# Kernel optimization log

Hardware: AMD Instinct MI355X
Metric: run time of the kernel (lower is better)

Reference implementation:

```python
import jax, jax.numpy as jnp
import numpy as np

B, D_IN, H, C = 8192, 3072, 2000, 10


def binarized(x):
    # deterministic Binarize: sign(x) scaled by mean |x| (matches quant_mode='det', allow_scale=True)
    return jnp.sign(x) * jnp.mean(jnp.abs(x))


def setup_inputs() -> dict:
    key = jax.random.key(0)
    ks = jax.random.split(key, 6)

    def lin(k, out_f, in_f):
        # torch nn.Linear default init: U(-1/sqrt(in_f), 1/sqrt(in_f))
        bound = 1.0 / np.sqrt(in_f)
        kw, kb = jax.random.split(k)
        W = jax.random.uniform(kw, (out_f, in_f), minval=-bound, maxval=bound, dtype=jnp.float32)
        b = jax.random.uniform(kb, (out_f,), minval=-bound, maxval=bound, dtype=jnp.float32)
        return W, b

    x = jax.random.normal(ks[0], (B, D_IN), dtype=jnp.float32)
    W1, b1 = lin(ks[1], H, D_IN)
    W2, b2 = lin(ks[2], H, H)
    W3, b3 = lin(ks[3], H, H)
    W4, b4 = lin(ks[4], H, H)
    W5, b5 = lin(ks[5], C, H)
    return {"x": x, "W1": W1, "b1": b1, "W2": W2, "b2": b2,
            "W3": W3, "b3": b3, "W4": W4, "b4": b4, "W5": W5, "b5": b5}


def reference(x, W1, b1, W2, b2, W3, b3, W4, b4, W5, b5):
    # layer 1: binary_a==1 but layer_index==1 -> input NOT binarized; weight binarized
    h = jax.nn.relu(x @ binarized(W1).T + b1)
    # layers 2-4: binarize both activations and weights
    h = jax.nn.relu(binarized(h) @ binarized(W2).T + b2)
    h = jax.nn.relu(binarized(h) @ binarized(W3).T + b3)
    h = jax.nn.relu(binarized(h) @ binarized(W4).T + b4)
    # fc1 is a plain fp32 Linear
    return h @ W5.T + b5
```

## Files before the change

kernel.cpp:

```cpp
#include <hip/hip_runtime.h>
#include <hip/hip_bf16.h>
#include <stdint.h>

typedef __bf16 bf16_t;
typedef __attribute__((ext_vector_type(8))) __bf16 bf16x8;
typedef __attribute__((ext_vector_type(4))) float f32x4;
typedef __attribute__((ext_vector_type(4))) int i32x4;
typedef __attribute__((ext_vector_type(8))) char i8x8;

#define GLD_LDS16(g, l) __builtin_amdgcn_global_load_lds( \
    (__attribute__((address_space(1))) void*)(g), \
    (__attribute__((address_space(3))) void*)(l), 16, 0, 0)

__device__ __forceinline__ void block_reduce_atomic_d(double v, double* dst) {
    #pragma unroll
    for (int off = 32; off > 0; off >>= 1) v += __shfl_down(v, off);
    __shared__ double rb[4];
    const int t = threadIdx.x;
    if ((t & 63) == 0) rb[t >> 6] = v;
    __syncthreads();
    if (t == 0) atomicAdd(dst, rb[0] + rb[1] + rb[2] + rb[3]);
}

__device__ __forceinline__ void prep_w1_row(
    const float* __restrict__ W, int r, bf16_t* __restrict__ S, double* sumOut)
{
    const int t = threadIdx.x;
    double sl = 0.0;
    for (int cb = t * 8; cb < 3072; cb += 2048) {
        bf16x8 o;
        if (r < 2000) {
            #pragma unroll
            for (int j = 0; j < 8; ++j) {
                float v = W[(size_t)r * 3072 + cb + j];
                sl += (double)fabsf(v);
                o[j] = (bf16_t)(v > 0.f ? 1.f : (v < 0.f ? -1.f : 0.f));
            }
        } else {
            #pragma unroll
            for (int j = 0; j < 8; ++j) o[j] = (bf16_t)0.f;
        }
        *(bf16x8*)&S[(size_t)r * 6144 + cb] = o;
        *(bf16x8*)&S[(size_t)r * 6144 + 3072 + cb] = o;
    }
    block_reduce_atomic_d(sl, sumOut);
}

__device__ __forceinline__ void prep_wi8_row(
    const float* __restrict__ W, int r, int8_t* __restrict__ S, double* sumOut)
{
    const int t = threadIdx.x;
    const int cb = t * 8;
    double sl = 0.0;
    i8x8 o;
    if (r < 2000) {
        #pragma unroll
        for (int j = 0; j < 8; ++j) {
            int c = cb + j;
            float v = (c < 2000) ? W[(size_t)r * 2000 + c] : 0.f;
            sl += (double)fabsf(v);
            o[j] = (char)(v > 0.f ? 1 : (v < 0.f ? -1 : 0));
        }
    } else {
        #pragma unroll
        for (int j = 0; j < 8; ++j) o[j] = 0;
    }
    *(i8x8*)&S[(size_t)r * 2048 + cb] = o;
    block_reduce_atomic_d(sl, sumOut);
}

__device__ __forceinline__ void prep_x_row(
    const float* __restrict__ x, int r, bf16_t* __restrict__ XLi, bf16_t* __restrict__ XLr)
{
    const int t = threadIdx.x;
    for (int cb = t * 8; cb < 3072; cb += 2048) {
        float4 v0 = *(const float4*)&x[(size_t)r * 3072 + cb];
        float4 v1 = *(const float4*)&x[(size_t)r * 3072 + cb + 4];
        float xv[8] = {v0.x, v0.y, v0.z, v0.w, v1.x, v1.y, v1.z, v1.w};
        bf16x8 hi, lo, re;
        #pragma unroll
        for (int j = 0; j < 8; ++j) {
            int Q = (int)lrintf(xv[j] * 16384.f);
            int d0 = ((Q + 256) & 511) - 256;
            int d1 = (Q - d0) / 512;
            float rr = xv[j] - (float)Q * (1.f / 16384.f);
            hi[j] = (bf16_t)(float)(d1 * 512);
            lo[j] = (bf16_t)(float)d0;
            re[j] = (bf16_t)(rr * 16384.f);
        }
        *(bf16x8*)&XLi[(size_t)r * 6144 + cb]        = hi;
        *(bf16x8*)&XLi[(size_t)r * 6144 + 3072 + cb] = lo;
        *(bf16x8*)&XLr[(size_t)r * 3072 + cb]        = re;
    }
}

__global__ __launch_bounds__(256) void prep_all(
    const float* __restrict__ W1, const float* __restrict__ W2,
    const float* __restrict__ W3, const float* __restrict__ W4,
    const float* __restrict__ x,
    bf16_t* __restrict__ sW1, int8_t* __restrict__ sW2,
    int8_t* __restrict__ sW3, int8_t* __restrict__ sW4,
    bf16_t* __restrict__ XLi, bf16_t* __restrict__ XLr,
    double* __restrict__ scD)
{
    const int g = blockIdx.x;
    if      (g < 2048)  prep_w1_row(W1, g, sW1, scD + 0);
    else if (g < 4096)  prep_wi8_row(W2, g - 2048, sW2, scD + 1);
    else if (g < 6144)  prep_wi8_row(W3, g - 4096, sW3, scD + 2);
    else if (g < 8192)  prep_wi8_row(W4, g - 6144, sW4, scD + 3);
    else                prep_x_row(x, g - 8192, XLi, XLr);
}

__global__ __launch_bounds__(256, 4) void gemm_bin(
    const bf16_t* __restrict__ A, const bf16_t* __restrict__ B, int K, int ldB,
    float* __restrict__ rawOut,
    const float* __restrict__ addPlane,
    const double* __restrict__ sumW, double invDivW, double extraScale,
    const float* __restrict__ bias,
    int8_t* __restrict__ binOut,
    double* __restrict__ habs)
{
    __shared__ __align__(16) bf16_t sA[128 * 64];
    __shared__ __align__(16) bf16_t sB[128 * 64];
    const int t = threadIdx.x;
    const int lane = t & 63;
    const int wave = t >> 6;
    const int wr = wave >> 1, wc = wave & 1;
    const int qa = lane >> 4, rA = lane & 15;
    const size_t bm = (size_t)blockIdx.y * 128, bn = (size_t)blockIdx.x * 128;

    f32x4 acc[4][4] = {};

    const bf16_t* Abase = A + bm * (size_t)K;
    const bf16_t* Bbase = B + bn * (size_t)ldB;

    const int swz = rA & 7;
    const int offk0 = ((0 + qa) ^ swz) * 8;
    const int offk1 = ((4 + qa) ^ swz) * 8;
    const int arow = wr * 64 + rA;
    const int brow = wc * 64 + rA;

    for (int k0 = 0; k0 < K; k0 += 64) {
        #pragma unroll
        for (int i = 0; i < 4; ++i) {
            int c = i * 256 + t;
            int row = c >> 3, cc = c & 7;
            int ccg = cc ^ (row & 7);
            GLD_LDS16(Abase + (size_t)row * K + k0 + ccg * 8, &sA[c * 8]);
        }
        #pragma unroll
        for (int i = 0; i < 4; ++i) {
            int c = i * 256 + t;
            int row = c >> 3, cc = c & 7;
            int ccg = cc ^ (row & 7);
            GLD_LDS16(Bbase + (size_t)row * ldB + k0 + ccg * 8, &sB[c * 8]);
        }
        __syncthreads();

        bf16x8 fa[4][2], fb[4][2];
        #pragma unroll
        for (int i = 0; i < 4; ++i) {
            fa[i][0] = *(const bf16x8*)&sA[(arow + i * 16) * 64 + offk0];
            fa[i][1] = *(const bf16x8*)&sA[(arow + i * 16) * 64 + offk1];
            fb[i][0] = *(const bf16x8*)&sB[(brow + i * 16) * 64 + offk0];
            fb[i][1] = *(const bf16x8*)&sB[(brow + i * 16) * 64 + offk1];
        }
        #pragma unroll
        for (int i = 0; i < 4; ++i)
            #pragma unroll
            for (int j = 0; j < 4; ++j) {
                acc[i][j] = __builtin_amdgcn_mfma_f32_16x16x32_bf16(fa[i][0], fb[j][0], acc[i][j], 0, 0, 0);
                acc[i][j] = __builtin_amdgcn_mfma_f32_16x16x32_bf16(fa[i][1], fb[j][1], acc[i][j], 0, 0, 0);
            }
        __syncthreads();
    }

    if (rawOut) {
        #pragma unroll
        for (int i = 0; i < 4; ++i)
            #pragma unroll
            for (int j = 0; j < 4; ++j)
                #pragma unroll
                for (int rr = 0; rr < 4; ++rr) {
                    int m = (int)bm + wr * 64 + i * 16 + qa * 4 + rr;
                    int n = (int)bn + wc * 64 + j * 16 + rA;
                    rawOut[(size_t)m * 2048 + n] = acc[i][j][rr];
                }
        return;
    }

    const double scale = sumW[0] * invDivW * extraScale;
    double hs = 0.0;
    #pragma unroll
    for (int i = 0; i < 4; ++i) {
        #pragma unroll
        for (int j = 0; j < 4; ++j) {
            #pragma unroll
            for (int rr = 0; rr < 4; ++rr) {
                int m = (int)bm + wr * 64 + i * 16 + qa * 4 + rr;
                int n = (int)bn + wc * 64 + j * 16 + rA;
                size_t idx = (size_t)m * 2048 + n;
                double s = (double)acc[i][j][rr];
                if (addPlane) s += (double)addPlane[idx];
                double z = s * scale + (n < 2000 ? (double)bias[n] : -1.0);
                binOut[idx] = (int8_t)(z > 0.0 ? 1 : 0);
                if (n < 2000 && z > 0.0) hs += z;
            }
        }
    }
    if (habs) block_reduce_atomic_d(hs, habs);
}

__global__ __launch_bounds__(256, 4) void gemm_i8(
    const int8_t* __restrict__ A, const int8_t* __restrict__ B,
    const double* __restrict__ sumW, double invDivW,
    const double* __restrict__ sumH, double invDivH,
    const float* __restrict__ bias,
    int8_t* __restrict__ binOut, bf16_t* __restrict__ hOut,
    double* __restrict__ habs)
{
    const int K = 2048;
    __shared__ __align__(16) int8_t sA[128 * 128];
    __shared__ __align__(16) int8_t sB[128 * 128];
    const int t = threadIdx.x;
    const int lane = t & 63;
    const int wave = t >> 6;
    const int wr = wave >> 1, wc = wave & 1;
    const int qa = lane >> 4, rA = lane & 15;
    const size_t bm = (size_t)blockIdx.y * 128, bn = (size_t)blockIdx.x * 128;

    i32x4 acc[4][4] = {};

    const int8_t* Abase = A + bm * (size_t)K;
    const int8_t* Bbase = B + bn * (size_t)K;

    const int swz = rA & 7;
    const int offb0 = ((0 + qa) ^ swz) * 16;
    const int offb1 = ((4 + qa) ^ swz) * 16;
    const int arow = wr * 64 + rA;
    const int brow = wc * 64 + rA;

    for (int k0 = 0; k0 < K; k0 += 128) {
        #pragma unroll
        for (int i = 0; i < 4; ++i) {
            int c = i * 256 + t;
            int row = c >> 3, cc = c & 7;
            int ccg = cc ^ (row & 7);
            GLD_LDS16(Abase + (size_t)row * K + k0 + ccg * 16, &sA[c * 16]);
        }
        #pragma unroll
        for (int i = 0; i < 4; ++i) {
            int c = i * 256 + t;
            int row = c >> 3, cc = c & 7;
            int ccg = cc ^ (row & 7);
            GLD_LDS16(Bbase + (size_t)row * K + k0 + ccg * 16, &sB[c * 16]);
        }
        __syncthreads();

        {
            i32x4 fa[4], fb[4];
            #pragma unroll
            for (int i = 0; i < 4; ++i) {
                fa[i] = *(const i32x4*)&sA[(arow + i * 16) * 128 + offb0];
                fb[i] = *(const i32x4*)&sB[(brow + i * 16) * 128 + offb0];
            }
            #pragma unroll
            for (int i = 0; i < 4; ++i)
                #pragma unroll
                for (int j = 0; j < 4; ++j)
                    acc[i][j] = __builtin_amdgcn_mfma_i32_16x16x64_i8(fa[i], fb[j], acc[i][j], 0, 0, 0);
        }
        {
            i32x4 fa[4], fb[4];
            #pragma unroll
            for (int i = 0; i < 4; ++i) {
                fa[i] = *(const i32x4*)&sA[(arow + i * 16) * 128 + offb1];
                fb[i] = *(const i32x4*)&sB[(brow + i * 16) * 128 + offb1];
            }
            #pragma unroll
            for (int i = 0; i < 4; ++i)
                #pragma unroll
                for (int j = 0; j < 4; ++j)
                    acc[i][j] = __builtin_amdgcn_mfma_i32_16x16x64_i8(fa[i], fb[j], acc[i][j], 0, 0, 0);
        }
        __syncthreads();
    }

    const double scale = sumW[0] * invDivW * sumH[0] * invDivH;
    double hs = 0.0;
    #pragma unroll
    for (int i = 0; i < 4; ++i) {
        #pragma unroll
        for (int j = 0; j < 4; ++j) {
            #pragma unroll
            for (int rr = 0; rr < 4; ++rr) {
                int m = (int)bm + wr * 64 + i * 16 + qa * 4 + rr;
                int n = (int)bn + wc * 64 + j * 16 + rA;
                size_t idx = (size_t)m * 2048 + n;
                double z = (double)acc[i][j][rr] * scale +
                           (n < 2000 ? (double)bias[n] : -1.0);
                if (binOut) binOut[idx] = (int8_t)(z > 0.0 ? 1 : 0);
                if (hOut)   hOut[idx] = (bf16_t)(float)(z > 0.0 ? z : 0.0);
                if (n < 2000 && z > 0.0) hs += z;
            }
        }
    }
    if (habs) block_reduce_atomic_d(hs, habs);
}

__global__ __launch_bounds__(256) void fc_final(
    const bf16_t* __restrict__ h4, const float* __restrict__ W5,
    const float* __restrict__ b5, float* __restrict__ out)
{
    const int r = blockIdx.x, t = threadIdx.x;
    float acc[10] = {};
    for (int k = t; k < 2000; k += 256) {
        float a = (float)h4[(size_t)r * 2048 + k];
        #pragma unroll
        for (int c = 0; c < 10; ++c) acc[c] += a * W5[c * 2000 + k];
    }
    __shared__ float red[4][10];
    #pragma unroll
    for (int c = 0; c < 10; ++c) {
        float v = acc[c];
        #pragma unroll
        for (int off = 32; off > 0; off >>= 1) v += __shfl_down(v, off);
        if ((t & 63) == 0) red[t >> 6][c] = v;
    }
    __syncthreads();
    if (t < 10) out[(size_t)r * 10 + t] = red[0][t] + red[1][t] + red[2][t] + red[3][t] + b5[t];
}

extern "C" void kernel_launch(void* const* d_in, const int* in_sizes, int n_in,
                              void* d_out, int out_size, void* d_ws, size_t ws_size,
                              hipStream_t stream)
{
    const float* x  = (const float*)d_in[0];
    const float* W1 = (const float*)d_in[1];
    const float* b1 = (const float*)d_in[2];
    const float* W2 = (const float*)d_in[3];
    const float* b2 = (const float*)d_in[4];
    const float* W3 = (const float*)d_in[5];
    const float* b3 = (const float*)d_in[6];
    const float* W4 = (const float*)d_in[7];
    const float* b4 = (const float*)d_in[8];
    const float* W5 = (const float*)d_in[9];
    const float* b5 = (const float*)d_in[10];
    float* out = (float*)d_out;
    (void)ws_size; (void)in_sizes; (void)n_in; (void)out_size;

    const size_t PH = (size_t)8192 * 2048;

    char* w = (char*)d_ws;
    double* scD = (double*)w;
    size_t off = 256;
    bf16_t* XLi = (bf16_t*)(w + off); off += (size_t)8192 * 6144 * 2;
    bf16_t* XLr = (bf16_t*)(w + off); off += (size_t)8192 * 3072 * 2;
    bf16_t* sW1 = (bf16_t*)(w + off); off += (size_t)2048 * 6144 * 2;
    float*  Ti  = (float*)(w + off);  off += PH * 4;
    int8_t* p0  = (int8_t*)(w + off); off += PH;
    int8_t* sW2 = (int8_t*)(w + off); off += (size_t)2048 * 2048;
    int8_t* sW3 = (int8_t*)(w + off); off += (size_t)2048 * 2048;
    int8_t* sW4 = (int8_t*)(w + off); off += (size_t)2048 * 2048;
    int8_t* p1  = (int8_t*)XLi;
    bf16_t* h4  = (bf16_t*)Ti;

    hipMemsetAsync(w, 0, 256, stream);
    prep_all<<<16384, 256, 0, stream>>>(W1, W2, W3, W4, x,
                                        sW1, sW2, sW3, sW4, XLi, XLr, scD);

    dim3 grid(16, 64), blk(256);
    gemm_bin<<<grid, blk, 0, stream>>>(XLi, sW1, 6144, 6144, Ti, nullptr,
                                       nullptr, 0.0, 1.0, nullptr, nullptr, nullptr);
    gemm_bin<<<grid, blk, 0, stream>>>(XLr, sW1, 3072, 6144, nullptr, Ti,
                                       scD + 0, 1.0 / 6144000.0, 1.0 / 16384.0,
                                       b1, p0, scD + 4);

    gemm_i8<<<grid, blk, 0, stream>>>(p0, sW2,
                                      scD + 1, 1.0 / 4000000.0, scD + 4, 1.0 / 16384000.0,
                                      b2, p1, nullptr, scD + 5);
    gemm_i8<<<grid, blk, 0, stream>>>(p1, sW3,
                                      scD + 2, 1.0 / 4000000.0, scD + 5, 1.0 / 16384000.0,
                                      b3, p0, nullptr, scD + 6);
    gemm_i8<<<grid, blk, 0, stream>>>(p0, sW4,
                                      scD + 3, 1.0 / 4000000.0, scD + 6, 1.0 / 16384000.0,
                                      b4, nullptr, h4, nullptr);
    fc_final<<<8192, 256, 0, stream>>>(h4, W5, b5, out);
}
```

Measured before the change: 856.9 us.

## Fuse layer-1 split-precision GEMMs into one kernel sharing the weight tile

Merges the two layer-1 GEMMs (hi/lo bf16 split against a duplicated sign-weight matrix, then a residual pass reading the fp32 intermediate) into one kernel. It loads the hi, lo and residual activation tiles together with a single copy of the sign-weight tile, and keeps two accumulators in registers. This drops the fp32 intermediate plane write and read, the duplicated weight storage, and one launch. In exchange it doubles accumulator registers, removes the occupancy hint, and uses a smaller K-step of 32 with more barriers per unit of work.

Measured after the change: 1.134 ms. 1.32x slower.

```diff
diff --git a/kernel.cpp b/kernel.cpp
--- a/kernel.cpp
+++ b/kernel.cpp
@@ -40,8 +40,7 @@
             #pragma unroll
             for (int j = 0; j < 8; ++j) o[j] = (bf16_t)0.f;
         }
-        *(bf16x8*)&S[(size_t)r * 6144 + cb] = o;
-        *(bf16x8*)&S[(size_t)r * 6144 + 3072 + cb] = o;
+        *(bf16x8*)&S[(size_t)r * 3072 + cb] = o;
     }
     block_reduce_atomic_d(sl, sumOut);
 }
@@ -111,17 +110,18 @@
     else                prep_x_row(x, g - 8192, XLi, XLr);
 }
 
-__global__ __launch_bounds__(256, 4) void gemm_bin(
-    const bf16_t* __restrict__ A, const bf16_t* __restrict__ B, int K, int ldB,
-    float* __restrict__ rawOut,
-    const float* __restrict__ addPlane,
-    const double* __restrict__ sumW, double invDivW, double extraScale,
+__global__ __launch_bounds__(256) void gemm_l1(
+    const bf16_t* __restrict__ XLi, const bf16_t* __restrict__ XLr,
+    const bf16_t* __restrict__ Bs,
+    const double* __restrict__ sumW,
     const float* __restrict__ bias,
     int8_t* __restrict__ binOut,
     double* __restrict__ habs)
 {
-    __shared__ __align__(16) bf16_t sA[128 * 64];
-    __shared__ __align__(16) bf16_t sB[128 * 64];
+    __shared__ __align__(16) bf16_t sHi[128 * 32];
+    __shared__ __align__(16) bf16_t sLo[128 * 32];
+    __shared__ __align__(16) bf16_t sRe[128 * 32];
+    __shared__ __align__(16) bf16_t sB [128 * 32];
     const int t = threadIdx.x;
     const int lane = t & 63;
     const int wave = t >> 6;
@@ -129,67 +129,72 @@
     const int qa = lane >> 4, rA = lane & 15;
     const size_t bm = (size_t)blockIdx.y * 128, bn = (size_t)blockIdx.x * 128;
 
-    f32x4 acc[4][4] = {};
-
-    const bf16_t* Abase = A + bm * (size_t)K;
-    const bf16_t* Bbase = B + bn * (size_t)ldB;
-
-    const int swz = rA & 7;
-    const int offk0 = ((0 + qa) ^ swz) * 8;
-    const int offk1 = ((4 + qa) ^ swz) * 8;
+    f32x4 accI[4][4] = {};
+    f32x4 accR[4][4] = {};
+
+    const bf16_t* HiB = XLi + bm * 6144;
+    const bf16_t* LoB = XLi + bm * 6144 + 3072;
+    const bf16_t* ReB = XLr + bm * 3072;
+    const bf16_t* BB  = Bs  + bn * 3072;
+
+    const int offk = (qa ^ (rA & 3)) * 8;
     const int arow = wr * 64 + rA;
     const int brow = wc * 64 + rA;
 
-    for (int k0 = 0; k0 < K; k0 += 64) {
-        #pragma unroll
-        for (int i = 0; i < 4; ++i) {
+    for (int k0 = 0; k0 < 3072; k0 += 32) {
+        #pragma unroll
+        for (int i = 0; i < 2; ++i) {
             int c = i * 256 + t;
-            int row = c >> 3, cc = c & 7;
-            int ccg = cc ^ (row & 7);
-            GLD_LDS16(Abase + (size_t)row * K + k0 + ccg * 8, &sA[c * 8]);
-        }
-        #pragma unroll
-        for (int i = 0; i < 4; ++i) {
-            int c = i * 256 + t;
-            int row = c >> 3, cc = c & 7;
-            int ccg = cc ^ (row & 7);
-            GLD_LDS16(Bbase + (size_t)row * ldB + k0 + ccg * 8, &sB[c * 8]);
+            int row = c >> 2, cc = c & 3;
+            int ccg = cc ^ (row & 3);
+            GLD_LDS16(HiB + (size_t)row * 6144 + k0 + ccg * 8, &sHi[c * 8]);
+            GLD_LDS16(LoB + (size_t)row * 6144 + k0 + ccg * 8, &sLo[c * 8]);
+            GLD_LDS16(ReB + (size_t)row * 3072 + k0 + ccg * 8, &sRe[c * 8]);
+            GLD_LDS16(BB  + (size_t)row * 3072 + k0 + ccg * 8, &sB [c * 8]);
         }
         __syncthreads();
 
-        bf16x8 fa[4][2], fb[4][2];
-        #pragma unroll
-        for (int i = 0; i < 4; ++i) {
-            fa[i][0] = *(const bf16x8*)&sA[(arow + i * 16) * 64 + offk0];
-            fa[i][1] = *(const bf16x8*)&sA[(arow + i * 16) * 64 + offk1];
-            fb[i][0] = *(const bf16x8*)&sB[(brow + i * 16) * 64 + offk0];
-            fb[i][1] = *(const bf16x8*)&sB[(brow + i * 16) * 64 + offk1];
-        }
-        #pragma unroll
-        for (int i = 0; i < 4; ++i)
-            #pragma unroll
-            for (int j = 0; j < 4; ++j) {
-                acc[i][j] = __builtin_amdgcn_mfma_f32_16x16x32_bf16(fa[i][0], fb[j][0], acc[i][j], 0, 0, 0);
-                acc[i][j] = __builtin_amdgcn_mfma_f32_16x16x32_bf16(fa[i][1], fb[j][1], acc[i][j], 0, 0, 0);
-            }
+        bf16x8 fb[4];
+        #pragma unroll
+        for (int j = 0; j < 4; ++j)
+            fb[j] = *(const bf16x8*)&sB[(brow + j * 16) * 32 + offk];
+        {
+            bf16x8 fa[4];
+            #pragma unroll
+            for (int i = 0; i < 4; ++i)
+                fa[i] = *(const bf16x8*)&sHi[(arow + i * 16) * 32 + offk];
+            #pragma unroll
+            for (int i = 0; i < 4; ++i)
+                #pragma unroll
+                for (int j = 0; j < 4; ++j)
+                    accI[i][j] = __builtin_amdgcn_mfma_f32_16x16x32_bf16(fa[i], fb[j], accI[i][j], 0, 0, 0);
+        }
+        {
+            bf16x8 fa[4];
+            #pragma unroll
+            for (int i = 0; i < 4; ++i)
+                fa[i] = *(const bf16x8*)&sLo[(arow + i * 16) * 32 + offk];
+            #pragma unroll
+            for (int i = 0; i < 4; ++i)
+                #pragma unroll
+                for (int j = 0; j < 4; ++j)
+                    accI[i][j] = __builtin_amdgcn_mfma_f32_16x16x32_bf16(fa[i], fb[j], accI[i][j], 0, 0, 0);
+        }
+        {
+            bf16x8 fa[4];
+            #pragma unroll
+            for (int i = 0; i < 4; ++i)
+                fa[i] = *(const bf16x8*)&sRe[(arow + i * 16) * 32 + offk];
+            #pragma unroll
+            for (int i = 0; i < 4; ++i)
+                #pragma unroll
+                for (int j = 0; j < 4; ++j)
+                    accR[i][j] = __builtin_amdgcn_mfma_f32_16x16x32_bf16(fa[i], fb[j], accR[i][j], 0, 0, 0);
+        }
         __syncthreads();
     }
 
-    if (rawOut) {
-        #pragma unroll
-        for (int i = 0; i < 4; ++i)
-            #pragma unroll
-            for (int j = 0; j < 4; ++j)
-                #pragma unroll
-                for (int rr = 0; rr < 4; ++rr) {
-                    int m = (int)bm + wr * 64 + i * 16 + qa * 4 + rr;
-                    int n = (int)bn + wc * 64 + j * 16 + rA;
-                    rawOut[(size_t)m * 2048 + n] = acc[i][j][rr];
-                }
-        return;
-    }
-
-    const double scale = sumW[0] * invDivW * extraScale;
+    const double scale = sumW[0] * (1.0 / 6144000.0) * (1.0 / 16384.0);
     double hs = 0.0;
     #pragma unroll
     for (int i = 0; i < 4; ++i) {
@@ -200,8 +205,7 @@
                 int m = (int)bm + wr * 64 + i * 16 + qa * 4 + rr;
                 int n = (int)bn + wc * 64 + j * 16 + rA;
                 size_t idx = (size_t)m * 2048 + n;
-                double s = (double)acc[i][j][rr];
-                if (addPlane) s += (double)addPlane[idx];
+                double s = (double)accR[i][j][rr] + (double)accI[i][j][rr];
                 double z = s * scale + (n < 2000 ? (double)bias[n] : -1.0);
                 binOut[idx] = (int8_t)(z > 0.0 ? 1 : 0);
                 if (n < 2000 && z > 0.0) hs += z;
@@ -370,11 +374,7 @@
                                         sW1, sW2, sW3, sW4, XLi, XLr, scD);
 
     dim3 grid(16, 64), blk(256);
-    gemm_bin<<<grid, blk, 0, stream>>>(XLi, sW1, 6144, 6144, Ti, nullptr,
-                                       nullptr, 0.0, 1.0, nullptr, nullptr, nullptr);
-    gemm_bin<<<grid, blk, 0, stream>>>(XLr, sW1, 3072, 6144, nullptr, Ti,
-                                       scD + 0, 1.0 / 6144000.0, 1.0 / 16384.0,
-                                       b1, p0, scD + 4);
+    gemm_l1<<<grid, blk, 0, stream>>>(XLi, XLr, sW1, scD + 0, b1, p0, scD + 4);
 
     gemm_i8<<<grid, blk, 0, stream>>>(p0, sW2,
                                       scD + 1, 1.0 / 4000000.0, scD + 4, 1.0 / 16384000.0,
```

## Add dedicated 256x256-tile pipelined bf16 GEMM for layer-1 main pass

Applied to the files above, without the earlier changes.

Replaces the generic 128x128 gemm_bin launch for the big K=6144 layer-1 GEMM with a specialized kernel that uses 512 threads, 256x256 output tiles, and double-buffered LDS staged via global_load_lds. Loads for the next k-tiles are interleaved with MFMA work in quarter steps, with explicit waitcnt/barrier and setprio scheduling, plus an XOR swizzle and block-index remap for L2 locality. The goal is more data reuse per loaded byte and better overlap of memory with compute. In exchange it uses much more LDS and registers per block, which limits occupancy, and the hardcoded sizes make it specific to this shape.

Result: faster. 804.0 us (-6.2%).

```diff
diff --git a/kernel.cpp b/kernel.cpp
--- a/kernel.cpp
+++ b/kernel.cpp
@@ -109,6 +109,109 @@
     else if (g < 6144)  prep_wi8_row(W3, g - 4096, sW3, scD + 2);
     else if (g < 8192)  prep_wi8_row(W4, g - 6144, sW4, scD + 3);
     else                prep_x_row(x, g - 8192, XLi, XLr);
+}
+
+__global__ __launch_bounds__(512, 2) void gemm_l1a8(
+    const bf16_t* __restrict__ A,
+    const bf16_t* __restrict__ B,
+    float* __restrict__ Ti)
+{
+    __shared__ __align__(16) bf16_t lds[2][2][2][128 * 64];
+    const int tid = threadIdx.x;
+    const int lane = tid & 63, wid = tid >> 6;
+    const int wr = wid >> 2, wc = wid & 3;
+    const int rA = lane & 15, qa = lane >> 4;
+
+    const int fid = (int)blockIdx.x;
+    const int sid = (fid & 7) * 32 + (fid >> 3);
+    const size_t bm = (size_t)(sid >> 3) * 256;
+    const size_t bn = (size_t)(sid & 7) * 256;
+
+    const bf16_t* Ab = A + bm * 6144;
+    const bf16_t* Bb = B + bn * 6144;
+
+    const int sr = tid >> 3;
+    const int sgoff = ((tid & 7) ^ (sr & 7)) * 8;
+    const int sdoff = tid * 8;
+
+#define STG(b_, o_, h_, r_, kt_) \
+    GLD_LDS16(((o_) ? Bb : Ab) + (size_t)((h_) * 128 + (r_) * 64 + sr) * 6144 \
+              + (kt_) * 64 + sgoff, \
+              &lds[b_][o_][h_][(r_) * 4096 + sdoff])
+
+    STG(0, 0, 0, 0, 0); STG(0, 0, 0, 1, 0); STG(0, 0, 1, 0, 0); STG(0, 0, 1, 1, 0);
+    STG(0, 1, 0, 0, 0); STG(0, 1, 0, 1, 0); STG(0, 1, 1, 0, 0); STG(0, 1, 1, 1, 0);
+    STG(1, 1, 0, 0, 1); STG(1, 1, 0, 1, 1); STG(1, 1, 1, 0, 1); STG(1, 1, 1, 1, 1);
+    STG(1, 0, 0, 0, 1); STG(1, 0, 1, 0, 1);
+    asm volatile("s_waitcnt vmcnt(6)" ::: "memory");
+    __builtin_amdgcn_s_barrier();
+
+    const int offk0 = ((0 + qa) ^ (rA & 7)) * 8;
+    const int offk1 = ((4 + qa) ^ (rA & 7)) * 8;
+    const int browb = (wc & 1) * 64;
+    const int bhalf = wc >> 1;
+
+    f32x4 acc[8][4] = {};
+
+    for (int t = 0; t < 96; ++t) {
+        const int p = t & 1;
+        const bf16_t* Al = lds[p][0][wr];
+        const bf16_t* Bl = lds[p][1][bhalf];
+
+        bf16x8 fb[4][2];
+        #pragma unroll
+        for (int q = 0; q < 4; ++q) {
+            if (q == 0) {
+                #pragma unroll
+                for (int n = 0; n < 4; ++n) {
+                    fb[n][0] = *(const bf16x8*)&Bl[(browb + n * 16 + rA) * 64 + offk0];
+                    fb[n][1] = *(const bf16x8*)&Bl[(browb + n * 16 + rA) * 64 + offk1];
+                }
+            }
+            bf16x8 fa[2][2];
+            #pragma unroll
+            for (int mm = 0; mm < 2; ++mm) {
+                fa[mm][0] = *(const bf16x8*)&Al[((q * 2 + mm) * 16 + rA) * 64 + offk0];
+                fa[mm][1] = *(const bf16x8*)&Al[((q * 2 + mm) * 16 + rA) * 64 + offk1];
+            }
+            if (q == 0) {
+                if (t < 95) { STG(p ^ 1, 0, 0, 1, t + 1); STG(p ^ 1, 0, 1, 1, t + 1); }
+            } else if (t < 94) {
+                if (q == 1)      { STG(p, 1, 0, 0, t + 2); STG(p, 1, 0, 1, t + 2); }
+                else if (q == 2) { STG(p, 1, 1, 0, t + 2); STG(p, 1, 1, 1, t + 2); }
+                else             { STG(p, 0, 0, 0, t + 2); STG(p, 0, 1, 0, t + 2); }
+            }
+            __builtin_amdgcn_s_barrier();
+            __builtin_amdgcn_s_setprio(1);
+            #pragma unroll
+            for (int mm = 0; mm < 2; ++mm)
+                #pragma unroll
+                for (int n = 0; n < 4; ++n) {
+                    acc[q * 2 + mm][n] = __builtin_amdgcn_mfma_f32_16x16x32_bf16(
+                        fa[mm][0], fb[n][0], acc[q * 2 + mm][n], 0, 0, 0);
+                    acc[q * 2 + mm][n] = __builtin_amdgcn_mfma_f32_16x16x32_bf16(
+                        fa[mm][1], fb[n][1], acc[q * 2 + mm][n], 0, 0, 0);
+                }
+            __builtin_amdgcn_s_setprio(0);
+            if (q == 3) {
+                if (t < 94) asm volatile("s_waitcnt vmcnt(6)" ::: "memory");
+                else        asm volatile("s_waitcnt vmcnt(0)" ::: "memory");
+            }
+            __builtin_amdgcn_s_barrier();
+        }
+    }
+#undef STG
+
+    #pragma unroll
+    for (int m = 0; m < 8; ++m)
+        #pragma unroll
+        for (int n = 0; n < 4; ++n)
+            #pragma unroll
+            for (int rr = 0; rr < 4; ++rr) {
+                size_t mm = bm + wr * 128 + m * 16 + qa * 4 + rr;
+                size_t nn = bn + wc * 64 + n * 16 + rA;
+                Ti[mm * 2048 + nn] = acc[m][n][rr];
+            }
 }
 
 __global__ __launch_bounds__(256, 4) void gemm_bin(
@@ -369,9 +472,9 @@
     prep_all<<<16384, 256, 0, stream>>>(W1, W2, W3, W4, x,
                                         sW1, sW2, sW3, sW4, XLi, XLr, scD);
 
+    gemm_l1a8<<<256, 512, 0, stream>>>(XLi, sW1, Ti);
+
     dim3 grid(16, 64), blk(256);
-    gemm_bin<<<grid, blk, 0, stream>>>(XLi, sW1, 6144, 6144, Ti, nullptr,
-                                       nullptr, 0.0, 1.0, nullptr, nullptr, nullptr);
     gemm_bin<<<grid, blk, 0, stream>>>(XLr, sW1, 3072, 6144, nullptr, Ti,
                                        scD + 0, 1.0 / 6144000.0, 1.0 / 16384.0,
                                        b1, p0, scD + 4);
```
